# Optimization experiments

Hardware: AMD Instinct MI355X
Metric: run time of the kernel (lower is better)

The kernel has to match this reference:

```python
import jax, jax.numpy as jnp
import numpy as np

NUM_HEAD = 16
MASKED_BIAS = -10000.0


def setup_inputs() -> dict:
    key = jax.random.key(0)
    k1, k2, k3 = jax.random.split(key, 3)
    B, M, N = 2, 2048, 1024
    x = jax.random.normal(k1, (B, M, N), dtype=jnp.float32)
    w_attn = jax.random.normal(k2, (N, 3 * N), dtype=jnp.float32) * 0.02
    w_proj = jax.random.normal(k3, (N, N), dtype=jnp.float32) * 0.02
    b_attn = jnp.zeros((3 * N,), dtype=jnp.float32)
    b_proj = jnp.zeros((N,), dtype=jnp.float32)
    return {"x": x, "w_attn": w_attn, "w_proj": w_proj,
            "b_attn": b_attn, "b_proj": b_proj}


def reference(x, w_attn, w_proj, b_attn, b_proj):
    B, M, N = x.shape
    H = NUM_HEAD
    d = N // H  # head dim
    # fused QKV projection: [B,M,3N]
    qkv = jnp.einsum('bmn,nd->bmd', x, w_attn) + b_attn
    q, k, v = jnp.split(qkv, 3, axis=-1)
    # split heads -> [B,H,M,d]
    q = q.reshape(B, M, H, d).transpose(0, 2, 1, 3)
    k = k.reshape(B, M, H, d).transpose(0, 2, 1, 3)
    v = v.reshape(B, M, H, d).transpose(0, 2, 1, 3)
    # scaled dot-product scores [B,H,M,M]
    scores = jnp.einsum('bhqd,bhkd->bhqk', q, k) / jnp.sqrt(jnp.float32(d))
    causal = jnp.tril(jnp.ones((M, M), dtype=bool))  # GPT-2 bias buffer
    scores = jnp.where(causal, scores, jnp.float32(MASKED_BIAS))
    attn = jax.nn.softmax(scores, axis=-1)
    # context [B,H,M,d] -> [B,M,N]
    ctx = jnp.einsum('bhqk,bhkd->bhqd', attn, v)
    ctx = ctx.transpose(0, 2, 1, 3).reshape(B, M, N)
    # output projection
    out = jnp.einsum('bmn,no->bmo', ctx, w_proj) + b_proj
    return out
```

## Files before the change

kernel.cpp:

```cpp
#include <hip/hip_runtime.h>

typedef __attribute__((ext_vector_type(8))) __bf16 bf16x8;
typedef __attribute__((ext_vector_type(4))) __bf16 bf16x4;
typedef __attribute__((ext_vector_type(4))) float f32x4;

__device__ __forceinline__ void async_copy16(const void* g, void* l) {
    __builtin_amdgcn_global_load_lds(
        (const __attribute__((address_space(1))) void*)g,
        (__attribute__((address_space(3))) void*)l, 16, 0, 0);
}

__device__ __forceinline__ float fexp2(float x) {
    return __builtin_amdgcn_exp2f(x);
}

__global__ __launch_bounds__(256) void prep_k(
    const float* __restrict__ x, __bf16* __restrict__ xb,
    const float* __restrict__ wa, __bf16* __restrict__ wAt,
    const float* __restrict__ wp, __bf16* __restrict__ wPt)
{
    __shared__ float tile[32][33];
    const int bx = blockIdx.x;
    if (bx < 2048) {
        size_t i = ((size_t)bx * 256 + threadIdx.x) * 8;
        float4 a = *(const float4*)&x[i];
        float4 b = *(const float4*)&x[i + 4];
        bf16x8 o;
        o[0] = (__bf16)a.x; o[1] = (__bf16)a.y; o[2] = (__bf16)a.z; o[3] = (__bf16)a.w;
        o[4] = (__bf16)b.x; o[5] = (__bf16)b.y; o[6] = (__bf16)b.z; o[7] = (__bf16)b.w;
        *(bf16x8*)&xb[i] = o;
        return;
    }
    const float* src; __bf16* dst; int R, C, c0, r0;
    if (bx < 5120) {
        int id = bx - 2048;
        src = wa; dst = wAt; R = 1024; C = 3072;
        c0 = (id % 96) * 32; r0 = (id / 96) * 32;
    } else {
        int id = bx - 5120;
        src = wp; dst = wPt; R = 1024; C = 1024;
        c0 = (id & 31) * 32; r0 = (id >> 5) * 32;
    }
    int tx = threadIdx.x & 31, ty = threadIdx.x >> 5;
    for (int i = ty; i < 32; i += 8)
        tile[i][tx] = src[(size_t)(r0 + i) * C + (c0 + tx)];
    __syncthreads();
    for (int i = ty; i < 32; i += 8)
        dst[(size_t)(c0 + i) * R + (r0 + tx)] = (__bf16)tile[tx][i];
}

template <int MODE, int TN>
__global__ __launch_bounds__(256) void gemm_bt(
    const __bf16* __restrict__ A, const __bf16* __restrict__ Bt,
    const float* __restrict__ bias, int K,
    __bf16* __restrict__ O0, __bf16* __restrict__ O1, __bf16* __restrict__ O2,
    float* __restrict__ Of)
{
    constexpr int NJ = TN / 32;
    __shared__ __align__(16) __bf16 lds_a[2][128 * 32];
    __shared__ __align__(16) __bf16 lds_b[2][TN * 32];
    const int row0 = blockIdx.x * 128;
    const int col0 = blockIdx.y * TN;
    const int tid  = threadIdx.x;
    const int lane = tid & 63;
    const int w    = tid >> 6;
    const int wm   = (w >> 1) * 64, wn = (w & 1) * (TN / 2);
    const int quad = lane >> 4, l16 = lane & 15;

    auto stage = [&](int pb, int kb) {
#pragma unroll
        for (int t = 0; t < 2; ++t) {
            int s = t * 256 + tid;
            int L = s >> 3, c = (s & 7) ^ (L & 7);
            int row = 2 * L + (c >> 2), ch = c & 3;
            async_copy16(&A[(size_t)(row0 + row) * K + kb + ch * 8],
                         (char*)&lds_a[pb][0] + (t * 256 + w * 64) * 16);
        }
#pragma unroll
        for (int t = 0; t < TN / 64; ++t) {
            int s = t * 256 + tid;
            int L = s >> 3, c = (s & 7) ^ (L & 7);
            int row = 2 * L + (c >> 2), ch = c & 3;
            async_copy16(&Bt[(size_t)(col0 + row) * K + kb + ch * 8],
                         (char*)&lds_b[pb][0] + (t * 256 + w * 64) * 16);
        }
    };

    const int nIter = K >> 5;
    f32x4 acc[4][NJ] = {};
    stage(0, 0);
    for (int it = 0; it < nIter; ++it) {
        __syncthreads();
        if (it + 1 < nIter) stage((it + 1) & 1, (it + 1) << 5);
        const __bf16* la = &lds_a[it & 1][0];
        const __bf16* lb = &lds_b[it & 1][0];
        bf16x8 af[4], bfr[NJ];
#pragma unroll
        for (int i = 0; i < 4; ++i) {
            int r = wm + i * 16 + l16;
            int L = r >> 1, g = ((r & 1) * 4 + quad) ^ (L & 7);
            af[i] = *(const bf16x8*)&la[L * 64 + g * 8];
        }
#pragma unroll
        for (int j = 0; j < NJ; ++j) {
            int r = wn + j * 16 + l16;
            int L = r >> 1, g = ((r & 1) * 4 + quad) ^ (L & 7);
            bfr[j] = *(const bf16x8*)&lb[L * 64 + g * 8];
        }
#pragma unroll
        for (int i = 0; i < 4; ++i)
#pragma unroll
            for (int j = 0; j < NJ; ++j)
                acc[i][j] = __builtin_amdgcn_mfma_f32_16x16x32_bf16(
                    af[i], bfr[j], acc[i][j], 0, 0, 0);
    }

#pragma unroll
    for (int i = 0; i < 4; ++i) {
        int grow = row0 + wm + i * 16 + quad * 4;
#pragma unroll
        for (int j = 0; j < NJ; ++j) {
            int gcol = col0 + wn + j * 16 + l16;
            float bv = bias[gcol];
            if constexpr (MODE == 0) {
                int which = gcol >> 10;
                int n  = gcol & 1023;
                int hh = n >> 6, dd = n & 63;
                int bb = grow >> 11, mm0 = grow & 2047;
                int bhh = bb * 16 + hh;
                if (which == 2) {
                    int w64 = mm0 & 63;
                    int mi = (mm0 & ~63) | (w64 & 32) | ((w64 & 12) << 1)
                             | ((w64 & 16) >> 2);
                    bf16x4 pk;
#pragma unroll
                    for (int r = 0; r < 4; ++r)
                        pk[r] = (__bf16)(acc[i][j][r] + bv);
                    *(bf16x4*)&O2[((size_t)bhh * 64 + dd) * 2048 + mi] = pk;
                } else {
#pragma unroll
                    for (int r = 0; r < 4; ++r) {
                        float v = acc[i][j][r] + bv;
                        if (which == 0)
                            O0[((size_t)bhh * 2048 + mm0 + r) * 64 + dd] =
                                (__bf16)(v * 0.18033688011112042f);
                        else
                            O1[((size_t)bhh * 2048 + mm0 + r) * 64 + dd] =
                                (__bf16)v;
                    }
                }
            } else {
#pragma unroll
                for (int r = 0; r < 4; ++r) {
                    int gr = grow + r;
                    Of[(size_t)gr * 1024 + gcol] = acc[i][j][r] + bv;
                }
            }
        }
    }
}

__global__ __launch_bounds__(256) void attn_kernel(
    const __bf16* __restrict__ Qh, const __bf16* __restrict__ Kh,
    const __bf16* __restrict__ Vt, __bf16* __restrict__ ctx)
{
    const int M = 2048, D = 64;
    const int bh = blockIdx.x;
    const int y  = blockIdx.y;
    const int b = bh >> 4, h = bh & 15;
    const int tid = threadIdx.x, lane = tid & 63, w = tid >> 6;
    const int quad = lane >> 4, l16 = lane & 15;

    const int nA = y + 1;
    const int nT = 33;
    const int qA0 = y * 64, qB0 = (31 - y) * 64;
    const int qwA = qA0 + w * 16, qwB = qB0 + w * 16;

    __shared__ __align__(16) __bf16 smem[2][2][64 * 64];

    const __bf16* Qp = Qh + (size_t)bh * M * D;
    const __bf16* Kp = Kh + (size_t)bh * M * D;
    const __bf16* Vp = Vt + (size_t)bh * D * M;

    bf16x8 qfA[2], qfB[2];
#pragma unroll
    for (int c = 0; c < 2; ++c) {
        qfA[c] = *(const bf16x8*)&Qp[(size_t)(qwA + l16) * D + c * 32 + quad * 8];
        qfB[c] = *(const bf16x8*)&Qp[(size_t)(qwB + l16) * D + c * 32 + quad * 8];
    }

    int ko[8];
#pragma unroll
    for (int t = 0; t < 4; ++t)
#pragma unroll
        for (int c = 0; c < 2; ++c) {
            int ch = ((c << 2) + quad) ^ (l16 & 7);
            ko[t * 2 + c] = (((t << 4) + l16) << 6) + (ch << 3);
        }
    int vo[8];
#pragma unroll
    for (int f = 0; f < 4; ++f)
#pragma unroll
        for (int tp = 0; tp < 2; ++tp) {
            int row = (f << 4) + l16;
            int g = ((tp << 2) + quad) ^ (row & 7);
            vo[f * 2 + tp] = (row << 6) + (g << 3);
        }

    const __bf16* kbase[2]; const __bf16* vbase[2];
    const __bf16* kg[2];    const __bf16* vg[2];
#pragma unroll
    for (int t = 0; t < 2; ++t) {
        int c = w * 128 + t * 64 + lane;
        int row = c >> 3, gch = (c & 7) ^ (row & 7);
        kbase[t] = &Kp[(size_t)row * 64 + gch * 8];
        vbase[t] = &Vp[(size_t)row * M + gch * 8];
        kg[t] = kbase[t]; vg[t] = vbase[t];
    }
    char* const lbase = (char*)smem + (w * 128) * 16;

    auto stage = [&](int pb) {
        char* d = lbase + pb * 16384;
#pragma unroll
        for (int t = 0; t < 2; ++t) {
            async_copy16(kg[t], d + t * 1024);
            async_copy16(vg[t], d + 8192 + t * 1024);
            kg[t] += 4096;
            vg[t] += 64;
        }
    };
    auto resetPtrs = [&]() {
#pragma unroll
        for (int t = 0; t < 2; ++t) { kg[t] = kbase[t]; vg[t] = vbase[t]; }
    };

    f32x4 accA[4] = {}, accB[4] = {};
    f32x4 acc_sA = {}, acc_sB = {};
    const __bf16 onev = (__bf16)1.0f;
    const bf16x8 ones8 = {onev, onev, onev, onev, onev, onev, onev, onev};

    auto compute = [&](const __bf16* kt, const __bf16* vt, int kb, int qw,
                       const bf16x8 (&qf)[2], f32x4 (&a2)[4], f32x4& as) {
        f32x4 s[4];
        __builtin_amdgcn_s_setprio(1);
#pragma unroll
        for (int t = 0; t < 4; ++t) {
            f32x4 tt = {};
#pragma unroll
            for (int c = 0; c < 2; ++c) {
                bf16x8 kf = *(const bf16x8*)(kt + ko[t * 2 + c]);
                tt = __builtin_amdgcn_mfma_f32_16x16x32_bf16(
                    kf, qf[c], tt, 0, 0, 0);
            }
            s[t] = tt;
        }
        __builtin_amdgcn_s_setprio(0);
        if (kb + 63 > qw) {
#pragma unroll
            for (int t = 0; t < 4; ++t)
#pragma unroll
                for (int r = 0; r < 4; ++r)
                    if (kb + t * 16 + quad * 4 + r > qw + l16)
                        s[t][r] = -1e30f;
        }
        bf16x8 pf[2];
#pragma unroll
        for (int tp = 0; tp < 2; ++tp) {
            bf16x8 pp;
#pragma unroll
            for (int r = 0; r < 4; ++r) {
                pp[r]     = (__bf16)fexp2(s[2 * tp][r]);
                pp[4 + r] = (__bf16)fexp2(s[2 * tp + 1][r]);
            }
            pf[tp] = pp;
        }
        __builtin_amdgcn_s_setprio(1);
#pragma unroll
        for (int f = 0; f < 4; ++f) {
#pragma unroll
            for (int tp = 0; tp < 2; ++tp) {
                bf16x8 vv = *(const bf16x8*)(vt + vo[f * 2 + tp]);
                a2[f] = __builtin_amdgcn_mfma_f32_16x16x32_bf16(
                    vv, pf[tp], a2[f], 0, 0, 0);
            }
        }
#pragma unroll
        for (int tp = 0; tp < 2; ++tp)
            as = __builtin_amdgcn_mfma_f32_16x16x32_bf16(
                ones8, pf[tp], as, 0, 0, 0);
        __builtin_amdgcn_s_setprio(0);
    };

    stage(0);
    if (nA == 1) resetPtrs();

    for (int it = 0; it < nT; ++it) {
        __syncthreads();
        int nxt = it + 1;
        if (nxt < nT) {
            stage(nxt & 1);
            if (nxt + 1 == nA) resetPtrs();
        }
        const __bf16* kt = &smem[it & 1][0][0];
        const __bf16* vt = &smem[it & 1][1][0];
        if (it < nA)
            compute(kt, vt, it * 64, qwA, qfA, accA, acc_sA);
        else
            compute(kt, vt, (it - nA) * 64, qwB, qfB, accB, acc_sB);
    }

    __bf16* ldsT = (__bf16*)smem;
    const int qq = tid >> 2;
    const int dp = (tid & 3) * 16;

    __syncthreads();
    {
        const float rinv = 1.0f / acc_sA[0];
#pragma unroll
        for (int f = 0; f < 4; ++f) {
            bf16x4 ov;
#pragma unroll
            for (int r = 0; r < 4; ++r)
                ov[r] = (__bf16)(accA[f][r] * rinv);
            *(bf16x4*)&ldsT[(w * 16 + l16) * 72 + f * 16 + quad * 4] = ov;
        }
        __syncthreads();
        const __bf16* src = &ldsT[qq * 72 + dp];
        __bf16* dst = &ctx[((size_t)(b * 2048 + qA0 + qq)) * 1024 + h * 64 + dp];
        *(bf16x8*)&dst[0] = *(const bf16x8*)&src[0];
        *(bf16x8*)&dst[8] = *(const bf16x8*)&src[8];
    }
    __syncthreads();
    {
        const float rinv = 1.0f / acc_sB[0];
#pragma unroll
        for (int f = 0; f < 4; ++f) {
            bf16x4 ov;
#pragma unroll
            for (int r = 0; r < 4; ++r)
                ov[r] = (__bf16)(accB[f][r] * rinv);
            *(bf16x4*)&ldsT[(w * 16 + l16) * 72 + f * 16 + quad * 4] = ov;
        }
        __syncthreads();
        const __bf16* src = &ldsT[qq * 72 + dp];
        __bf16* dst = &ctx[((size_t)(b * 2048 + qB0 + qq)) * 1024 + h * 64 + dp];
        *(bf16x8*)&dst[0] = *(const bf16x8*)&src[0];
        *(bf16x8*)&dst[8] = *(const bf16x8*)&src[8];
    }
}

extern "C" void kernel_launch(void* const* d_in, const int* in_sizes, int n_in,
                              void* d_out, int out_size, void* d_ws, size_t ws_size,
                              hipStream_t stream) {
    const float* x      = (const float*)d_in[0];
    const float* w_attn = (const float*)d_in[1];
    const float* w_proj = (const float*)d_in[2];
    const float* b_attn = (const float*)d_in[3];
    const float* b_proj = (const float*)d_in[4];
    float* out = (float*)d_out;

    char* ws = (char*)d_ws;
    __bf16* xb  = (__bf16*)(ws);
    __bf16* ctx = (__bf16*)(ws);
    __bf16* wAt = (__bf16*)(ws + 8388608);
    __bf16* wPt = (__bf16*)(ws + 14680064);
    __bf16* Vt  = (__bf16*)(ws + 16777216);
    __bf16* Qh  = (__bf16*)d_out;
    __bf16* Kh  = (__bf16*)d_out + 4194304;

    prep_k<<<6144, 256, 0, stream>>>(x, xb, w_attn, wAt, w_proj, wPt);
    gemm_bt<0, 128><<<dim3(32, 24), 256, 0, stream>>>(xb, wAt, b_attn, 1024,
                                                      Qh, Kh, Vt, nullptr);
    attn_kernel<<<dim3(32, 16), 256, 0, stream>>>(Qh, Kh, Vt, ctx);
    gemm_bt<1, 64><<<dim3(32, 16), 256, 0, stream>>>(ctx, wPt, b_proj, 1024,
                                                     nullptr, nullptr, nullptr, out);
}
```

Baseline: 173.7 us.

## Fuse fp32-to-bf16 conversion of x into the QKV GEMM A-tile load

Drops the separate x conversion pass from the prep kernel. The QKV GEMM now reads fp32 x straight from global memory into registers, converts to bf16, and writes the swizzled LDS tile after the current iteration's MFMAs, so the load overlaps compute. This removes one full write and re-read of a bf16 copy of x. In exchange each GEMM column block re-reads fp32 A (twice the bytes of bf16, once per 24 column tiles) through synchronous register loads rather than async LDS copies, and register pressure rises.

```diff
diff --git a/kernel.cpp b/kernel.cpp
--- a/kernel.cpp
+++ b/kernel.cpp
@@ -15,29 +15,17 @@
 }
 
 __global__ __launch_bounds__(256) void prep_k(
-    const float* __restrict__ x, __bf16* __restrict__ xb,
     const float* __restrict__ wa, __bf16* __restrict__ wAt,
     const float* __restrict__ wp, __bf16* __restrict__ wPt)
 {
     __shared__ float tile[32][33];
     const int bx = blockIdx.x;
-    if (bx < 2048) {
-        size_t i = ((size_t)bx * 256 + threadIdx.x) * 8;
-        float4 a = *(const float4*)&x[i];
-        float4 b = *(const float4*)&x[i + 4];
-        bf16x8 o;
-        o[0] = (__bf16)a.x; o[1] = (__bf16)a.y; o[2] = (__bf16)a.z; o[3] = (__bf16)a.w;
-        o[4] = (__bf16)b.x; o[5] = (__bf16)b.y; o[6] = (__bf16)b.z; o[7] = (__bf16)b.w;
-        *(bf16x8*)&xb[i] = o;
-        return;
-    }
     const float* src; __bf16* dst; int R, C, c0, r0;
-    if (bx < 5120) {
-        int id = bx - 2048;
+    if (bx < 3072) {
         src = wa; dst = wAt; R = 1024; C = 3072;
-        c0 = (id % 96) * 32; r0 = (id / 96) * 32;
+        c0 = (bx % 96) * 32; r0 = (bx / 96) * 32;
     } else {
-        int id = bx - 5120;
+        int id = bx - 3072;
         src = wp; dst = wPt; R = 1024; C = 1024;
         c0 = (id & 31) * 32; r0 = (id >> 5) * 32;
     }
@@ -49,9 +37,10 @@
         dst[(size_t)(c0 + i) * R + (r0 + tx)] = (__bf16)tile[tx][i];
 }
 
-template <int MODE, int TN>
+template <int MODE, int TN, bool AF32>
 __global__ __launch_bounds__(256) void gemm_bt(
-    const __bf16* __restrict__ A, const __bf16* __restrict__ Bt,
+    const __bf16* __restrict__ A, const float* __restrict__ Ax,
+    const __bf16* __restrict__ Bt,
     const float* __restrict__ bias, int K,
     __bf16* __restrict__ O0, __bf16* __restrict__ O1, __bf16* __restrict__ O2,
     float* __restrict__ Of)
@@ -67,7 +56,17 @@
     const int wm   = (w >> 1) * 64, wn = (w & 1) * (TN / 2);
     const int quad = lane >> 4, l16 = lane & 15;
 
-    auto stage = [&](int pb, int kb) {
+    auto stageB = [&](int pb, int kb) {
+#pragma unroll
+        for (int t = 0; t < TN / 64; ++t) {
+            int s = t * 256 + tid;
+            int L = s >> 3, c = (s & 7) ^ (L & 7);
+            int row = 2 * L + (c >> 2), ch = c & 3;
+            async_copy16(&Bt[(size_t)(col0 + row) * K + kb + ch * 8],
+                         (char*)&lds_b[pb][0] + (t * 256 + w * 64) * 16);
+        }
+    };
+    auto stageA_lds = [&](int pb, int kb) {
 #pragma unroll
         for (int t = 0; t < 2; ++t) {
             int s = t * 256 + tid;
@@ -76,22 +75,52 @@
             async_copy16(&A[(size_t)(row0 + row) * K + kb + ch * 8],
                          (char*)&lds_a[pb][0] + (t * 256 + w * 64) * 16);
         }
-#pragma unroll
-        for (int t = 0; t < TN / 64; ++t) {
+    };
+    auto loadA_f32 = [&](float4 (&ar)[2][2], int kb) {
+#pragma unroll
+        for (int t = 0; t < 2; ++t) {
             int s = t * 256 + tid;
             int L = s >> 3, c = (s & 7) ^ (L & 7);
             int row = 2 * L + (c >> 2), ch = c & 3;
-            async_copy16(&Bt[(size_t)(col0 + row) * K + kb + ch * 8],
-                         (char*)&lds_b[pb][0] + (t * 256 + w * 64) * 16);
+            const float* sp = &Ax[(size_t)(row0 + row) * K + kb + ch * 8];
+            ar[t][0] = *(const float4*)sp;
+            ar[t][1] = *(const float4*)(sp + 4);
+        }
+    };
+    auto writeA_f32 = [&](const float4 (&ar)[2][2], int pb) {
+#pragma unroll
+        for (int t = 0; t < 2; ++t) {
+            int s = t * 256 + tid;
+            bf16x8 o;
+            o[0] = (__bf16)ar[t][0].x; o[1] = (__bf16)ar[t][0].y;
+            o[2] = (__bf16)ar[t][0].z; o[3] = (__bf16)ar[t][0].w;
+            o[4] = (__bf16)ar[t][1].x; o[5] = (__bf16)ar[t][1].y;
+            o[6] = (__bf16)ar[t][1].z; o[7] = (__bf16)ar[t][1].w;
+            *(bf16x8*)((char*)&lds_a[pb][0] + (size_t)s * 16) = o;
         }
     };
 
     const int nIter = K >> 5;
     f32x4 acc[4][NJ] = {};
-    stage(0, 0);
+    if constexpr (AF32) {
+        float4 ar0[2][2];
+        loadA_f32(ar0, 0);
+        stageB(0, 0);
+        writeA_f32(ar0, 0);
+    } else {
+        stageA_lds(0, 0);
+        stageB(0, 0);
+    }
     for (int it = 0; it < nIter; ++it) {
         __syncthreads();
-        if (it + 1 < nIter) stage((it + 1) & 1, (it + 1) << 5);
+        const int nxt = it + 1;
+        const bool pre = nxt < nIter;
+        float4 ar[2][2];
+        if (pre) {
+            if constexpr (AF32) loadA_f32(ar, nxt << 5);
+            else                stageA_lds(nxt & 1, nxt << 5);
+            stageB(nxt & 1, nxt << 5);
+        }
         const __bf16* la = &lds_a[it & 1][0];
         const __bf16* lb = &lds_b[it & 1][0];
         bf16x8 af[4], bfr[NJ];
@@ -113,6 +142,9 @@
             for (int j = 0; j < NJ; ++j)
                 acc[i][j] = __builtin_amdgcn_mfma_f32_16x16x32_bf16(
                     af[i], bfr[j], acc[i][j], 0, 0, 0);
+        if constexpr (AF32) {
+            if (pre) writeA_f32(ar, nxt & 1);
+        }
     }
 
 #pragma unroll
@@ -360,7 +392,6 @@
     float* out = (float*)d_out;
 
     char* ws = (char*)d_ws;
-    __bf16* xb  = (__bf16*)(ws);
     __bf16* ctx = (__bf16*)(ws);
     __bf16* wAt = (__bf16*)(ws + 8388608);
     __bf16* wPt = (__bf16*)(ws + 14680064);
@@ -368,10 +399,10 @@
     __bf16* Qh  = (__bf16*)d_out;
     __bf16* Kh  = (__bf16*)d_out + 4194304;
 
-    prep_k<<<6144, 256, 0, stream>>>(x, xb, w_attn, wAt, w_proj, wPt);
-    gemm_bt<0, 128><<<dim3(32, 24), 256, 0, stream>>>(xb, wAt, b_attn, 1024,
-                                                      Qh, Kh, Vt, nullptr);
+    prep_k<<<4096, 256, 0, stream>>>(w_attn, wAt, w_proj, wPt);
+    gemm_bt<0, 128, true><<<dim3(32, 24), 256, 0, stream>>>(
+        nullptr, x, wAt, b_attn, 1024, Qh, Kh, Vt, nullptr);
     attn_kernel<<<dim3(32, 16), 256, 0, stream>>>(Qh, Kh, Vt, ctx);
-    gemm_bt<1, 64><<<dim3(32, 16), 256, 0, stream>>>(ctx, wPt, b_proj, 1024,
-                                                     nullptr, nullptr, nullptr, out);
-}
+    gemm_bt<1, 64, false><<<dim3(32, 16), 256, 0, stream>>>(
+        ctx, nullptr, wPt, b_proj, 1024, nullptr, nullptr, nullptr, out);
+}
```

New measurement: 182.4 us. 1.05x slower.
